# Kernel optimization log

Hardware: AMD Instinct MI355X
Metric: run time of the kernel (lower is better)

The kernel has to match this reference:

```python
import jax, jax.numpy as jnp
import numpy as np

B = 131072
IN_FEAT = 128
OUT_FEAT = 128
RANK = 32


def setup_inputs() -> dict:
    key = jax.random.key(0)
    k1, k2, k3, k4, k5 = jax.random.split(key, 5)
    inp = jax.random.normal(k1, (B, IN_FEAT), dtype=jnp.float32)
    # per-sample generated weight flattened [B, r*r], as passed to set_parameters
    gen_weight = jax.random.normal(k2, (B, RANK * RANK), dtype=jnp.float32) * 0.05
    U = jax.random.normal(k3, (IN_FEAT, RANK), dtype=jnp.float32) * (1.0 / np.sqrt(IN_FEAT))
    V = jax.random.normal(k4, (RANK, OUT_FEAT), dtype=jnp.float32) * (1.0 / np.sqrt(RANK))
    bias = jax.random.normal(k5, (OUT_FEAT,), dtype=jnp.float32) * 0.01
    return {"inp": inp, "gen_weight": gen_weight, "U": U, "V": V, "bias": bias}


def reference(inp, gen_weight, U, V, bias):
    # U_matrix projection: [B, I] -> [B, r]
    h = inp @ U
    # per-sample generated weight: [B, r*r] -> [B, r, r]
    W = gen_weight.reshape(-1, RANK, RANK)
    # (h.unsqueeze(-1) * W).sum(-2) == batched GEMV: [B, r]
    h = jnp.einsum('bi,bio->bo', h, W)
    # V_matrix projection + bias: [B, r] -> [B, O]
    out = h @ V + bias
    return out
```

## Files before the change

### kernel.cpp

```cpp
#include <hip/hip_runtime.h>


constexpr int RANK  = 32;
constexpr int BLOCK = 256;
constexpr int WPB   = BLOCK / 64;
constexpr int GRID  = 1024;
constexpr int NWAVES = GRID * WPB;

typedef int    i2_t __attribute__((ext_vector_type(2)));
typedef __fp16 h2_t __attribute__((ext_vector_type(2)));

#define USE_DOT2 (__has_builtin(__builtin_amdgcn_fdot2) && __has_builtin(__builtin_amdgcn_cvt_pkrtz))

__device__ __forceinline__ float red_xor8(float v) {
#if __has_builtin(__builtin_amdgcn_update_dpp)
    int m = __builtin_amdgcn_update_dpp(0, __float_as_int(v), 0x128, 0xf, 0xf, true);
    return v + __int_as_float(m);
#else
    return v + __shfl_xor(v, 8, 64);
#endif
}
__device__ __forceinline__ float red_xor16(float v) {
#if __has_builtin(__builtin_amdgcn_permlane16_swap)
    i2_t r = __builtin_amdgcn_permlane16_swap(__float_as_int(v), __float_as_int(v),
                                              false, false);
    return __int_as_float(r.x) + __int_as_float(r.y);
#else
    return v + __shfl_xor(v, 16, 64);
#endif
}
__device__ __forceinline__ float red_xor32(float v) {
#if __has_builtin(__builtin_amdgcn_permlane32_swap)
    i2_t r = __builtin_amdgcn_permlane32_swap(__float_as_int(v), __float_as_int(v),
                                              false, false);
    return __int_as_float(r.x) + __int_as_float(r.y);
#else
    return v + __shfl_xor(v, 32, 64);
#endif
}
__device__ __forceinline__ float red_g(float v) {
    return red_xor32(red_xor16(red_xor8(v)));
}

__device__ __forceinline__ h2_t rl_h2(int packed, int srclane) {
    int i = __builtin_amdgcn_readlane(packed, srclane);
    h2_t r; __builtin_memcpy(&r, &i, 4);
    return r;
}
__device__ __forceinline__ int pack_h2(float a, float b) {
#if USE_DOT2
    auto p = __builtin_amdgcn_cvt_pkrtz(a, b);
    int i; __builtin_memcpy(&i, &p, 4);
    return i;
#else
    return 0;
#endif
}

__global__ __launch_bounds__(BLOCK, 4)
void apg_linear_kernel(const float* __restrict__ inp,
                       const float* __restrict__ gw,
                       const float* __restrict__ U,
                       const float* __restrict__ V,
                       const float* __restrict__ bias,
                       float* __restrict__ out,
                       int nrows)
{
    __shared__ float4 u4s[1024];
    __shared__ float  hbuf[WPB][RANK];

    const int tid  = threadIdx.x;
    const int lane = tid & 63;
    const int wid  = tid >> 6;
    const int g    = lane >> 3;

    #pragma unroll
    for (int j = 0; j < 4; ++j)
        u4s[j * BLOCK + tid] = reinterpret_cast<const float4*>(U)[j * BLOCK + tid];
    __syncthreads();

#if USE_DOT2
    h2_t v2a[16], v2b[16];
    #pragma unroll
    for (int s = 0; s < 16; ++s) {
        const float2 r0 = reinterpret_cast<const float2*>(V + (2*s)     * 128)[lane];
        const float2 r1 = reinterpret_cast<const float2*>(V + (2*s + 1) * 128)[lane];
        v2a[s] = h2_t{(__fp16)r0.x, (__fp16)r1.x};
        v2b[s] = h2_t{(__fp16)r0.y, (__fp16)r1.y};
    }
#else
    float2 v2[RANK];
    #pragma unroll
    for (int r = 0; r < RANK; ++r)
        v2[r] = reinterpret_cast<const float2*>(V + r * 128)[lane];
#endif
    const float2 b2 = reinterpret_cast<const float2*>(bias)[lane];

    float* hw = hbuf[wid];

    const int wave0 = blockIdx.x * WPB + wid;
    const int iters = (nrows + NWAVES - 1) / NWAVES;

    float  x0A = 0.f, x1A = 0.f, x0B = 0.f, x1B = 0.f;
    float4 wA[4] = {}, wB[4] = {};

    const int rA0 = wave0;
    const int rB0 = wave0 + NWAVES;
    if (rA0 < nrows) {
        x0A = inp[rA0 * 128 + lane];
        x1A = inp[rA0 * 128 + 64 + lane];
        const float4* wp = reinterpret_cast<const float4*>(gw) + rA0 * 256;
        #pragma unroll
        for (int t = 0; t < 4; ++t) wA[t] = wp[t * 64 + lane];
    }
    if (rB0 < nrows) {
        x0B = inp[rB0 * 128 + lane];
        x1B = inp[rB0 * 128 + 64 + lane];
        const float4* wp = reinterpret_cast<const float4*>(gw) + rB0 * 256;
        #pragma unroll
        for (int t = 0; t < 4; ++t) wB[t] = wp[t * 64 + lane];
    }

    auto process = [&](int row, float& x0, float& x1, float4 (&w4)[4], int prow) {
        float h1a[4] = {0.f, 0.f, 0.f, 0.f};
        #pragma unroll
        for (int t = 0; t < 16; ++t) {
            const float xs = (t < 8) ? x0 : x1;
            const float xi = __shfl(xs, (t & 7) * 8 + g, 64);
            const float4 u = u4s[t * 64 + lane];
            h1a[0] = fmaf(xi, u.x, h1a[0]);
            h1a[1] = fmaf(xi, u.y, h1a[1]);
            h1a[2] = fmaf(xi, u.z, h1a[2]);
            h1a[3] = fmaf(xi, u.w, h1a[3]);
        }
        #pragma unroll
        for (int k = 0; k < 4; ++k) h1a[k] = red_g(h1a[k]);
        if (lane < 8)
            reinterpret_cast<float4*>(hw)[lane] =
                make_float4(h1a[0], h1a[1], h1a[2], h1a[3]);

        float h2a[4] = {0.f, 0.f, 0.f, 0.f};
        #pragma unroll
        for (int t = 0; t < 4; ++t) {
            const float hi = hw[t * 8 + g];
            h2a[0] = fmaf(hi, w4[t].x, h2a[0]);
            h2a[1] = fmaf(hi, w4[t].y, h2a[1]);
            h2a[2] = fmaf(hi, w4[t].z, h2a[2]);
            h2a[3] = fmaf(hi, w4[t].w, h2a[3]);
        }

        if (prow < nrows) {
            x0 = inp[prow * 128 + lane];
            x1 = inp[prow * 128 + 64 + lane];
            const float4* wp = reinterpret_cast<const float4*>(gw) + prow * 256;
            #pragma unroll
            for (int t = 0; t < 4; ++t) w4[t] = wp[t * 64 + lane];
        }

        #pragma unroll
        for (int k = 0; k < 4; ++k) h2a[k] = red_g(h2a[k]);

        float o0 = b2.x, o1 = b2.y;
#if USE_DOT2
        const int h2p0 = pack_h2(h2a[0], h2a[1]);
        const int h2p1 = pack_h2(h2a[2], h2a[3]);
        #pragma unroll
        for (int c = 0; c < 8; ++c) {
            const h2_t p0 = rl_h2(h2p0, c);
            const h2_t p1 = rl_h2(h2p1, c);
            o0 = __builtin_amdgcn_fdot2(p0, v2a[2*c],     o0, false);
            o1 = __builtin_amdgcn_fdot2(p0, v2b[2*c],     o1, false);
            o0 = __builtin_amdgcn_fdot2(p1, v2a[2*c + 1], o0, false);
            o1 = __builtin_amdgcn_fdot2(p1, v2b[2*c + 1], o1, false);
        }
#else
        #pragma unroll
        for (int r = 0; r < RANK; ++r) {
            const float h2r = __uint_as_float(
                __builtin_amdgcn_readlane(__float_as_uint(h2a[r & 3]), r >> 2));
            o0 = fmaf(h2r, v2[r].x, o0);
            o1 = fmaf(h2r, v2[r].y, o1);
        }
#endif
        reinterpret_cast<float2*>(out)[row * 64 + lane] = make_float2(o0, o1);
    };

    for (int it = 0; it < iters; it += 2) {
        const int rowA = wave0 + it * NWAVES;
        const int rowB = rowA + NWAVES;
        if (rowA >= nrows) break;
        process(rowA, x0A, x1A, wA, rowA + 2 * NWAVES);
        if (rowB >= nrows) break;
        process(rowB, x0B, x1B, wB, rowB + 2 * NWAVES);
    }
}

extern "C" void kernel_launch(void* const* d_in, const int* in_sizes, int n_in,
                              void* d_out, int out_size, void* d_ws, size_t ws_size,
                              hipStream_t stream)
{
    const float* inp  = (const float*)d_in[0];
    const float* gw   = (const float*)d_in[1];
    const float* U    = (const float*)d_in[2];
    const float* V    = (const float*)d_in[3];
    const float* bias = (const float*)d_in[4];
    float* out = (float*)d_out;
    const int nrows = in_sizes[0] / 128;

    apg_linear_kernel<<<GRID, BLOCK, 0, stream>>>(inp, gw, U, V, bias, out, nrows);
}
```

Baseline: 141.1 us.

## Process row pairs jointly with interleaved compute and full-pair prefetch

Restructures the per-wave loop so rows A and B are computed together: the shuffles, FMAs, reductions and dot2 chains for both rows are interleaved for more instruction-level parallelism, and both rows of the next pair are prefetched at the top of the iteration. Each row gets its own LDS buffer, and launch bounds drop to 2 blocks per SIMD so the extra registers fit. The loop count now assumes nrows divides evenly by 2*NWAVES with no tail handling, which is true for this input size but drops generality. Lower occupancy is the risk.

```diff
diff --git a/kernel.cpp b/kernel.cpp
--- a/kernel.cpp
+++ b/kernel.cpp
@@ -57,7 +57,7 @@
 #endif
 }
 
-__global__ __launch_bounds__(BLOCK, 4)
+__global__ __launch_bounds__(BLOCK, 2)
 void apg_linear_kernel(const float* __restrict__ inp,
                        const float* __restrict__ gw,
                        const float* __restrict__ U,
@@ -67,7 +67,7 @@
                        int nrows)
 {
     __shared__ float4 u4s[1024];
-    __shared__ float  hbuf[WPB][RANK];
+    __shared__ float  hbuf[WPB][2][RANK];
 
     const int tid  = threadIdx.x;
     const int lane = tid & 63;
@@ -96,102 +96,115 @@
 #endif
     const float2 b2 = reinterpret_cast<const float2*>(bias)[lane];
 
-    float* hw = hbuf[wid];
+    float* hwA = hbuf[wid][0];
+    float* hwB = hbuf[wid][1];
 
     const int wave0 = blockIdx.x * WPB + wid;
-    const int iters = (nrows + NWAVES - 1) / NWAVES;
-
-    float  x0A = 0.f, x1A = 0.f, x0B = 0.f, x1B = 0.f;
-    float4 wA[4] = {}, wB[4] = {};
-
-    const int rA0 = wave0;
-    const int rB0 = wave0 + NWAVES;
-    if (rA0 < nrows) {
-        x0A = inp[rA0 * 128 + lane];
-        x1A = inp[rA0 * 128 + 64 + lane];
-        const float4* wp = reinterpret_cast<const float4*>(gw) + rA0 * 256;
-        #pragma unroll
-        for (int t = 0; t < 4; ++t) wA[t] = wp[t * 64 + lane];
+    const int pairs = (nrows / NWAVES) / 2;
+
+    int rA = wave0, rB = wave0 + NWAVES;
+    float  xA0n = 0.f, xA1n = 0.f, xB0n = 0.f, xB1n = 0.f;
+    float4 wAn[4] = {}, wBn[4] = {};
+    {
+        xA0n = inp[rA * 128 + lane];
+        xA1n = inp[rA * 128 + 64 + lane];
+        const float4* wpA = reinterpret_cast<const float4*>(gw) + rA * 256;
+        #pragma unroll
+        for (int t = 0; t < 4; ++t) wAn[t] = wpA[t * 64 + lane];
+        xB0n = inp[rB * 128 + lane];
+        xB1n = inp[rB * 128 + 64 + lane];
+        const float4* wpB = reinterpret_cast<const float4*>(gw) + rB * 256;
+        #pragma unroll
+        for (int t = 0; t < 4; ++t) wBn[t] = wpB[t * 64 + lane];
     }
-    if (rB0 < nrows) {
-        x0B = inp[rB0 * 128 + lane];
-        x1B = inp[rB0 * 128 + 64 + lane];
-        const float4* wp = reinterpret_cast<const float4*>(gw) + rB0 * 256;
-        #pragma unroll
-        for (int t = 0; t < 4; ++t) wB[t] = wp[t * 64 + lane];
-    }
-
-    auto process = [&](int row, float& x0, float& x1, float4 (&w4)[4], int prow) {
-        float h1a[4] = {0.f, 0.f, 0.f, 0.f};
+
+    for (int it = 0; it < pairs; ++it) {
+        const float xA0 = xA0n, xA1 = xA1n, xB0 = xB0n, xB1 = xB1n;
+        float4 wA[4], wB[4];
+        #pragma unroll
+        for (int t = 0; t < 4; ++t) { wA[t] = wAn[t]; wB[t] = wBn[t]; }
+        const int rowA = rA, rowB = rB;
+
+        rA += 2 * NWAVES; rB += 2 * NWAVES;
+        if (it + 1 < pairs) {
+            xA0n = inp[rA * 128 + lane];
+            xA1n = inp[rA * 128 + 64 + lane];
+            const float4* wpA = reinterpret_cast<const float4*>(gw) + rA * 256;
+            #pragma unroll
+            for (int t = 0; t < 4; ++t) wAn[t] = wpA[t * 64 + lane];
+            xB0n = inp[rB * 128 + lane];
+            xB1n = inp[rB * 128 + 64 + lane];
+            const float4* wpB = reinterpret_cast<const float4*>(gw) + rB * 256;
+            #pragma unroll
+            for (int t = 0; t < 4; ++t) wBn[t] = wpB[t * 64 + lane];
+        }
+
+        float hA[4] = {0.f, 0.f, 0.f, 0.f};
+        float hB[4] = {0.f, 0.f, 0.f, 0.f};
         #pragma unroll
         for (int t = 0; t < 16; ++t) {
-            const float xs = (t < 8) ? x0 : x1;
-            const float xi = __shfl(xs, (t & 7) * 8 + g, 64);
-            const float4 u = u4s[t * 64 + lane];
-            h1a[0] = fmaf(xi, u.x, h1a[0]);
-            h1a[1] = fmaf(xi, u.y, h1a[1]);
-            h1a[2] = fmaf(xi, u.z, h1a[2]);
-            h1a[3] = fmaf(xi, u.w, h1a[3]);
-        }
-        #pragma unroll
-        for (int k = 0; k < 4; ++k) h1a[k] = red_g(h1a[k]);
-        if (lane < 8)
-            reinterpret_cast<float4*>(hw)[lane] =
-                make_float4(h1a[0], h1a[1], h1a[2], h1a[3]);
-
-        float h2a[4] = {0.f, 0.f, 0.f, 0.f};
+            const float4 u  = u4s[t * 64 + lane];
+            const float xsA = (t < 8) ? xA0 : xA1;
+            const float xsB = (t < 8) ? xB0 : xB1;
+            const int   src = (t & 7) * 8 + g;
+            const float xiA = __shfl(xsA, src, 64);
+            const float xiB = __shfl(xsB, src, 64);
+            hA[0] = fmaf(xiA, u.x, hA[0]);  hB[0] = fmaf(xiB, u.x, hB[0]);
+            hA[1] = fmaf(xiA, u.y, hA[1]);  hB[1] = fmaf(xiB, u.y, hB[1]);
+            hA[2] = fmaf(xiA, u.z, hA[2]);  hB[2] = fmaf(xiB, u.z, hB[2]);
+            hA[3] = fmaf(xiA, u.w, hA[3]);  hB[3] = fmaf(xiB, u.w, hB[3]);
+        }
+        #pragma unroll
+        for (int k = 0; k < 4; ++k) { hA[k] = red_g(hA[k]); hB[k] = red_g(hB[k]); }
+        if (lane < 8) {
+            reinterpret_cast<float4*>(hwA)[lane] = make_float4(hA[0], hA[1], hA[2], hA[3]);
+            reinterpret_cast<float4*>(hwB)[lane] = make_float4(hB[0], hB[1], hB[2], hB[3]);
+        }
+
+        float h2A[4] = {0.f, 0.f, 0.f, 0.f};
+        float h2B[4] = {0.f, 0.f, 0.f, 0.f};
         #pragma unroll
         for (int t = 0; t < 4; ++t) {
-            const float hi = hw[t * 8 + g];
-            h2a[0] = fmaf(hi, w4[t].x, h2a[0]);
-            h2a[1] = fmaf(hi, w4[t].y, h2a[1]);
-            h2a[2] = fmaf(hi, w4[t].z, h2a[2]);
-            h2a[3] = fmaf(hi, w4[t].w, h2a[3]);
-        }
-
-        if (prow < nrows) {
-            x0 = inp[prow * 128 + lane];
-            x1 = inp[prow * 128 + 64 + lane];
-            const float4* wp = reinterpret_cast<const float4*>(gw) + prow * 256;
-            #pragma unroll
-            for (int t = 0; t < 4; ++t) w4[t] = wp[t * 64 + lane];
-        }
-
-        #pragma unroll
-        for (int k = 0; k < 4; ++k) h2a[k] = red_g(h2a[k]);
-
-        float o0 = b2.x, o1 = b2.y;
+            const float hiA = hwA[t * 8 + g];
+            const float hiB = hwB[t * 8 + g];
+            h2A[0] = fmaf(hiA, wA[t].x, h2A[0]);  h2B[0] = fmaf(hiB, wB[t].x, h2B[0]);
+            h2A[1] = fmaf(hiA, wA[t].y, h2A[1]);  h2B[1] = fmaf(hiB, wB[t].y, h2B[1]);
+            h2A[2] = fmaf(hiA, wA[t].z, h2A[2]);  h2B[2] = fmaf(hiB, wB[t].z, h2B[2]);
+            h2A[3] = fmaf(hiA, wA[t].w, h2A[3]);  h2B[3] = fmaf(hiB, wB[t].w, h2B[3]);
+        }
+        #pragma unroll
+        for (int k = 0; k < 4; ++k) { h2A[k] = red_g(h2A[k]); h2B[k] = red_g(h2B[k]); }
+
+        float oA0 = b2.x, oA1 = b2.y, oB0 = b2.x, oB1 = b2.y;
 #if USE_DOT2
-        const int h2p0 = pack_h2(h2a[0], h2a[1]);
-        const int h2p1 = pack_h2(h2a[2], h2a[3]);
+        const int pA0 = pack_h2(h2A[0], h2A[1]), pA1 = pack_h2(h2A[2], h2A[3]);
+        const int pB0 = pack_h2(h2B[0], h2B[1]), pB1 = pack_h2(h2B[2], h2B[3]);
         #pragma unroll
         for (int c = 0; c < 8; ++c) {
-            const h2_t p0 = rl_h2(h2p0, c);
-            const h2_t p1 = rl_h2(h2p1, c);
-            o0 = __builtin_amdgcn_fdot2(p0, v2a[2*c],     o0, false);
-            o1 = __builtin_amdgcn_fdot2(p0, v2b[2*c],     o1, false);
-            o0 = __builtin_amdgcn_fdot2(p1, v2a[2*c + 1], o0, false);
-            o1 = __builtin_amdgcn_fdot2(p1, v2b[2*c + 1], o1, false);
+            const h2_t a0 = rl_h2(pA0, c), a1 = rl_h2(pA1, c);
+            const h2_t q0 = rl_h2(pB0, c), q1 = rl_h2(pB1, c);
+            oA0 = __builtin_amdgcn_fdot2(a0, v2a[2*c],     oA0, false);
+            oA1 = __builtin_amdgcn_fdot2(a0, v2b[2*c],     oA1, false);
+            oA0 = __builtin_amdgcn_fdot2(a1, v2a[2*c + 1], oA0, false);
+            oA1 = __builtin_amdgcn_fdot2(a1, v2b[2*c + 1], oA1, false);
+            oB0 = __builtin_amdgcn_fdot2(q0, v2a[2*c],     oB0, false);
+            oB1 = __builtin_amdgcn_fdot2(q0, v2b[2*c],     oB1, false);
+            oB0 = __builtin_amdgcn_fdot2(q1, v2a[2*c + 1], oB0, false);
+            oB1 = __builtin_amdgcn_fdot2(q1, v2b[2*c + 1], oB1, false);
         }
 #else
         #pragma unroll
         for (int r = 0; r < RANK; ++r) {
-            const float h2r = __uint_as_float(
-                __builtin_amdgcn_readlane(__float_as_uint(h2a[r & 3]), r >> 2));
-            o0 = fmaf(h2r, v2[r].x, o0);
-            o1 = fmaf(h2r, v2[r].y, o1);
-        }
-#endif
-        reinterpret_cast<float2*>(out)[row * 64 + lane] = make_float2(o0, o1);
-    };
-
-    for (int it = 0; it < iters; it += 2) {
-        const int rowA = wave0 + it * NWAVES;
-        const int rowB = rowA + NWAVES;
-        if (rowA >= nrows) break;
-        process(rowA, x0A, x1A, wA, rowA + 2 * NWAVES);
-        if (rowB >= nrows) break;
-        process(rowB, x0B, x1B, wB, rowB + 2 * NWAVES);
+            const float hAr = __uint_as_float(
+                __builtin_amdgcn_readlane(__float_as_uint(h2A[r & 3]), r >> 2));
+            const float hBr = __uint_as_float(
+                __builtin_amdgcn_readlane(__float_as_uint(h2B[r & 3]), r >> 2));
+            oA0 = fmaf(hAr, v2[r].x, oA0);  oA1 = fmaf(hAr, v2[r].y, oA1);
+            oB0 = fmaf(hBr, v2[r].x, oB0);  oB1 = fmaf(hBr, v2[r].y, oB1);
+        }
+#endif
+        reinterpret_cast<float2*>(out)[rowA * 64 + lane] = make_float2(oA0, oA1);
+        reinterpret_cast<float2*>(out)[rowB * 64 + lane] = make_float2(oB0, oB1);
     }
 }
 
```

After: 141.2 us. No clear change (+0.0%).
